# Optimization experiments

Measured on AMD Instinct MI355X. Metric: run time of the kernel, lower is better.

## Reference

```python
import jax, jax.numpy as jnp
import numpy as np

N_LAYER, N_HEAD, D_MODEL, D_FF = 6, 16, 1024, 4096
D_HEAD = D_MODEL // N_HEAD            # 64
M_FEAT = 2 * D_MODEL // N_HEAD        # 128, favor_feature_dims default
CHUNK = 128                           # chunk size for causal linear attention
LN_EPS = 1e-5
ATT_EPS = 1e-6                        # fast-transformers CausalLinearAttention eps
B, S = 4, 2048


def _layer_norm(x, g, b):
    mu = x.mean(-1, keepdims=True)
    var = ((x - mu) ** 2).mean(-1, keepdims=True)
    return (x - mu) * jax.lax.rsqrt(var + LN_EPS) * g + b


def _favor_phi(x, omega):
    # x: [B,H,S,Dh]; omega: [Dh, M//2]. FAVOR positive (hyperbolic) random
    # features: phi(x) = [exp(u - |x|^2/2), exp(-u - |x|^2/2)] / sqrt(M),
    # with x pre-scaled by sqrt(softmax_temp), softmax_temp = 1/sqrt(Dh).
    x = x * (D_HEAD ** -0.25)
    u = jnp.einsum('bhsd,dm->bhsm', x, omega)
    nrm = 0.5 * jnp.sum(x * x, axis=-1, keepdims=True)
    phi = jnp.concatenate([jnp.exp(u - nrm), jnp.exp(-u - nrm)], axis=-1)
    return phi * (M_FEAT ** -0.5)


def _causal_linear_attention(Qp, Kp, V):
    # Qp,Kp: [B,H,S,M] nonnegative features; V: [B,H,S,Dh].
    # out_i = phi(q_i)^T S_i / (phi(q_i)^T Z_i + eps),
    # S_i = sum_{j<=i} phi(k_j) v_j^T, Z_i = sum_{j<=i} phi(k_j).
    # Chunked: exclusive chunk prefix sums + masked intra-chunk matmul.
    b, h, s, m = Qp.shape
    d = V.shape[-1]
    c = s // CHUNK
    Qc = Qp.reshape(b, h, c, CHUNK, m)
    Kc = Kp.reshape(b, h, c, CHUNK, m)
    Vc = V.reshape(b, h, c, CHUNK, d)
    kv = jnp.einsum('bhclm,bhcld->bhcmd', Kc, Vc)   # per-chunk K^T V
    ksum = Kc.sum(axis=3)                            # [b,h,c,m]
    kv_pre = jnp.cumsum(kv, axis=2) - kv             # exclusive prefix over chunks
    ks_pre = jnp.cumsum(ksum, axis=2) - ksum
    scores = jnp.einsum('bhcim,bhcjm->bhcij', Qc, Kc)
    mask = jnp.tril(jnp.ones((CHUNK, CHUNK), bool))
    scores = jnp.where(mask, scores, 0.0)            # causal within chunk
    num = (jnp.einsum('bhcij,bhcjd->bhcid', scores, Vc)
           + jnp.einsum('bhcim,bhcmd->bhcid', Qc, kv_pre))
    den = scores.sum(-1) + jnp.einsum('bhcim,bhcm->bhci', Qc, ks_pre)
    out = num / (den[..., None] + ATT_EPS)
    return out.reshape(b, h, s, d)


def _forward(x, Wq, bq, Wk, bk, Wv, bv, Wo, bo, omega,
             g1, be1, W1, bf1, W2, bf2, g2, be2):
    bsz, slen, _ = x.shape
    out = x
    for l in range(N_LAYER):
        def proj(W, bvec):
            y = jnp.einsum('bsd,de->bse', out, W) + bvec
            return y.reshape(bsz, slen, N_HEAD, D_HEAD).transpose(0, 2, 1, 3)
        q = proj(Wq[l], bq[l])
        k = proj(Wk[l], bk[l])
        v = proj(Wv[l], bv[l])
        Qp = _favor_phi(q, omega[l])
        Kp = _favor_phi(k, omega[l])
        a = _causal_linear_attention(Qp, Kp, v)
        a = a.transpose(0, 2, 1, 3).reshape(bsz, slen, D_MODEL)
        a = jnp.einsum('bsd,de->bse', a, Wo[l]) + bo[l]
        h1 = _layer_norm(out + a, g1[l], be1[l])          # post-norm residual 1
        y = jax.nn.relu(jnp.einsum('bsd,df->bsf', h1, W1[l]) + bf1[l])
        y = jnp.einsum('bsf,fd->bsd', y, W2[l]) + bf2[l]
        out = _layer_norm(h1 + y, g2[l], be2[l])          # post-norm residual 2
    return out


def setup_inputs() -> dict:
    key = jax.random.key(0)
    ks = jax.random.split(key, 12)
    s = D_MODEL ** -0.5
    f32 = jnp.float32
    return {
        "x": jax.random.normal(ks[0], (B, S, D_MODEL), f32),
        "Wq": jax.random.normal(ks[1], (N_LAYER, D_MODEL, D_MODEL), f32) * s,
        "bq": jnp.zeros((N_LAYER, D_MODEL), f32),
        "Wk": jax.random.normal(ks[2], (N_LAYER, D_MODEL, D_MODEL), f32) * s,
        "bk": jnp.zeros((N_LAYER, D_MODEL), f32),
        "Wv": jax.random.normal(ks[3], (N_LAYER, D_MODEL, D_MODEL), f32) * s,
        "bv": jnp.zeros((N_LAYER, D_MODEL), f32),
        "Wo": jax.random.normal(ks[4], (N_LAYER, D_MODEL, D_MODEL), f32) * s,
        "bo": jnp.zeros((N_LAYER, D_MODEL), f32),
        "omega": jax.random.normal(ks[5], (N_LAYER, D_HEAD, M_FEAT // 2), f32),
        "g1": jnp.ones((N_LAYER, D_MODEL), f32),
        "be1": jnp.zeros((N_LAYER, D_MODEL), f32),
        "W1": jax.random.normal(ks[6], (N_LAYER, D_MODEL, D_FF), f32) * s,
        "bf1": jnp.zeros((N_LAYER, D_FF), f32),
        "W2": jax.random.normal(ks[7], (N_LAYER, D_FF, D_MODEL), f32) * (D_FF ** -0.5),
        "bf2": jnp.zeros((N_LAYER, D_MODEL), f32),
        "g2": jnp.ones((N_LAYER, D_MODEL), f32),
        "be2": jnp.zeros((N_LAYER, D_MODEL), f32),
    }


def reference(x, Wq, bq, Wk, bk, Wv, bv, Wo, bo, omega,
              g1, be1, W1, bf1, W2, bf2, g2, be2):
    return _forward(x, Wq, bq, Wk, bk, Wv, bv, Wo, bo, omega,
                    g1, be1, W1, bf1, W2, bf2, g2, be2)
```

## Files before the change

### kernel.cpp

```cpp
#include <hip/hip_runtime.h>

typedef unsigned short u16;
typedef __attribute__((ext_vector_type(8))) short bf16x8;
typedef __attribute__((ext_vector_type(4))) float f32x4;

#define DEV __device__ __forceinline__

DEV float b2f(u16 h){ return __uint_as_float(((unsigned)h) << 16); }
DEV u16 f2b(float f){ unsigned u = __float_as_uint(f); u += 0x7FFFu + ((u >> 16) & 1u); return (u16)(u >> 16); }

DEV void gload16(const u16* g, u16* l){
  __builtin_amdgcn_global_load_lds((const __attribute__((address_space(1))) unsigned*)g,
                                   (__attribute__((address_space(3))) unsigned*)l, 16, 0, 0);
}

__global__ __launch_bounds__(256) void wtrans7(const float* __restrict__ Wq, const float* __restrict__ Wk,
                                               const float* __restrict__ Wv, const float* __restrict__ Wo,
                                               const float* __restrict__ W1, const float* __restrict__ W2,
                                               const float* __restrict__ om,
                                               u16* __restrict__ Wcat, u16* __restrict__ Wot,
                                               u16* __restrict__ W1t, u16* __restrict__ W2t,
                                               u16* __restrict__ omT){
  __shared__ float tile[32][33];
  int id = blockIdx.x;
  const float* src; u16* dst; int K, N, kb, nb; float scale = 1.f;
  if (id < 4096){
    int wsel = id >> 10, loc = id & 1023;
    kb = loc >> 5; nb = loc & 31; K = 1024; N = 1024;
    src = (wsel == 0) ? Wq : (wsel == 1) ? Wk : (wsel == 2) ? Wv : Wo;
    dst = (wsel < 3) ? Wcat + (size_t)wsel * 1048576 : Wot;
  } else if (id < 8192){
    int loc = id - 4096;
    kb = loc & 31; nb = loc >> 5; K = 1024; N = 4096;
    src = W1; dst = W1t;
  } else if (id < 12288){
    int loc = id - 8192;
    kb = loc & 127; nb = loc >> 7; K = 4096; N = 1024;
    src = W2; dst = W2t;
  } else {
    int loc = id - 12288;
    kb = loc & 1; nb = loc >> 1; K = 64; N = 64;
    src = om; dst = omT; scale = 0.35355339059327373f;
  }
  int k0 = kb * 32, n0 = nb * 32;
  int tid = threadIdx.x;
#pragma unroll
  for (int i = 0; i < 4; i++){
    int idx = tid + i * 256;
    int r = idx >> 5, c = idx & 31;
    tile[r][c] = src[(size_t)(k0 + r) * N + n0 + c];
  }
  __syncthreads();
#pragma unroll
  for (int i = 0; i < 4; i++){
    int idx = tid + i * 256;
    int r = idx >> 5, c = idx & 31;
    dst[(size_t)(n0 + r) * K + k0 + c] = f2b(tile[c][r] * scale);
  }
}

__global__ __launch_bounds__(256) void cvt16(const float* __restrict__ src, u16* __restrict__ dst){
  size_t i = ((size_t)blockIdx.x * 256 + threadIdx.x) * 4;
  float4 f = *(const float4*)(src + i);
  ushort4 o = make_ushort4(f2b(f.x), f2b(f.y), f2b(f.z), f2b(f.w));
  *(ushort4*)(dst + i) = o;
}

__global__ void catbias(const float* __restrict__ bq, const float* __restrict__ bk,
                        const float* __restrict__ bv, float* __restrict__ bcat){
  int i = blockIdx.x * 256 + threadIdx.x;
  if (i >= 6 * 3072) return;
  int l = i / 3072, j = i % 3072;
  float v = (j < 1024) ? bq[l * 1024 + j] : (j < 2048) ? bk[l * 1024 + j - 1024] : bv[l * 1024 + j - 2048];
  bcat[i] = v;
}

__global__ void fillv(float* __restrict__ p, float v, int n){
  int i = blockIdx.x * 256 + threadIdx.x;
  if (i < n) p[i] = v;
}

DEV int swz(int r){ return (r & 3) ^ ((r >> 2) & 3); }

template<int EPI>
__global__ __launch_bounds__(256) void gemm_bt(const u16* __restrict__ A, const u16* __restrict__ Bt,
                                               const float* __restrict__ bias, void* __restrict__ outp,
                                               int M, int N, int K, int ldA, int ldB){
  __shared__ __align__(16) u16 As[2][4096];
  __shared__ __align__(16) u16 Bs[2][4096];
  const int tid = threadIdx.x;
  const int lane = tid & 63;
  const int w = tid >> 6;
  const int wm = w >> 1, wn = w & 1;
  int nx = gridDim.x;
  int nwg = nx * gridDim.y;
  int lin = blockIdx.y * nx + blockIdx.x;
  int cpx = nwg >> 3;
  int sw = (lin & 7) * cpx + (lin >> 3);
  const int m0 = (sw / nx) * 128;
  const int n0 = (sw % nx) * 128;

  int r0 = tid >> 2, c0 = tid & 3;
  int r1 = r0 + 64;
  int cs0 = c0 ^ swz(r0);
  int cs1 = c0 ^ swz(r1);
  const u16* ag0 = A + (size_t)(m0 + r0) * ldA + cs0 * 8;
  const u16* ag1 = A + (size_t)(m0 + r1) * ldA + cs1 * 8;
  const u16* bg0 = Bt + (size_t)(n0 + r0) * ldB + cs0 * 8;
  const u16* bg1 = Bt + (size_t)(n0 + r1) * ldB + cs1 * 8;

  f32x4 acc[4][4] = {};
  const int KT = K >> 5;

  gload16(ag0, &As[0][w * 512]);
  gload16(ag1, &As[0][2048 + w * 512]);
  gload16(bg0, &Bs[0][w * 512]);
  gload16(bg1, &Bs[0][2048 + w * 512]);

  for (int kt = 0; kt < KT; kt++){
    int cur = kt & 1;
    if (kt + 1 < KT){
      int ko = (kt + 1) << 5;
      gload16(ag0 + ko, &As[cur ^ 1][w * 512]);
      gload16(ag1 + ko, &As[cur ^ 1][2048 + w * 512]);
      gload16(bg0 + ko, &Bs[cur ^ 1][w * 512]);
      gload16(bg1 + ko, &Bs[cur ^ 1][2048 + w * 512]);
      asm volatile("s_waitcnt vmcnt(4)" ::: "memory");
    } else {
      asm volatile("s_waitcnt vmcnt(0)" ::: "memory");
    }
    __builtin_amdgcn_s_barrier();
    bf16x8 fa[4], fb[4];
#pragma unroll
    for (int m = 0; m < 4; m++){
      int row = wm * 64 + m * 16 + (lane & 15);
      int cc = (lane >> 4) ^ swz(row);
      fa[m] = *(const bf16x8*)(&As[cur][row * 32 + cc * 8]);
    }
#pragma unroll
    for (int n = 0; n < 4; n++){
      int row = wn * 64 + n * 16 + (lane & 15);
      int cc = (lane >> 4) ^ swz(row);
      fb[n] = *(const bf16x8*)(&Bs[cur][row * 32 + cc * 8]);
    }
#pragma unroll
    for (int m = 0; m < 4; m++)
#pragma unroll
      for (int n = 0; n < 4; n++)
        acc[m][n] = __builtin_amdgcn_mfma_f32_16x16x32_bf16(fa[m], fb[n], acc[m][n], 0, 0, 0);
    asm volatile("s_waitcnt lgkmcnt(0)" ::: "memory");
    __builtin_amdgcn_s_barrier();
  }

#pragma unroll
  for (int m = 0; m < 4; m++){
    int rowb = m0 + wm * 64 + m * 16 + ((lane >> 4) << 2);
#pragma unroll
    for (int n = 0; n < 4; n++){
      int col = n0 + wn * 64 + n * 16 + (lane & 15);
      float bv = bias[col];
      if (EPI == 5 && col >= 2048){
        int cv = col - 2048, hh = cv >> 6, dh = cv & 63;
        int bIdx = rowb >> 11, s4 = rowb & 2047;
        ushort4 pk = make_ushort4(f2b(acc[m][n][0] + bv), f2b(acc[m][n][1] + bv),
                                  f2b(acc[m][n][2] + bv), f2b(acc[m][n][3] + bv));
        *(ushort4*)&((u16*)outp + 16777216)[((size_t)(bIdx * 16 + hh) * 64 + dh) * 2048 + s4] = pk;
      } else {
#pragma unroll
        for (int r = 0; r < 4; r++){
          float v = acc[m][n][r] + bv;
          int rr = rowb + r;
          if (EPI == 5){
            u16* dst0 = (u16*)outp + (col < 1024 ? 0 : 8388608);
            int cv = col & 1023, hh = cv >> 6, dh = cv & 63;
            int bIdx = rr >> 11, s = rr & 2047;
            dst0[(((size_t)(bIdx * 16 + hh) * 2048 + s) << 6) + dh] = f2b(v);
          } else if (EPI == 2){
            ((u16*)outp)[(size_t)rr * N + col] = f2b(v > 0.f ? v : 0.f);
          } else {
            ((u16*)outp)[(size_t)rr * N + col] = f2b(v);
          }
        }
      }
    }
  }
}

template<int EPI>
__global__ __launch_bounds__(512, 1) void gemm8p(const u16* __restrict__ A, const u16* __restrict__ Bt,
                                                 const float* __restrict__ bias, void* __restrict__ outp,
                                                 int M, int N, int K, int ldA, int ldB){
  __shared__ __align__(16) u16 As[2][16384];
  __shared__ __align__(16) u16 Bs[2][16384];
  const int tid = threadIdx.x;
  const int lane = tid & 63;
  const int w = tid >> 6;
  const int wm = w >> 2, wn = w & 3;
  int nx = gridDim.x;
  int nwg = nx * gridDim.y;
  int lin = blockIdx.y * nx + blockIdx.x;
  int cpx = nwg >> 3;
  int sw = (lin & 7) * cpx + (lin >> 3);
  const int m0 = (sw / nx) * 256;
  const int n0 = (sw % nx) * 256;

  const int id1 = 512 + tid;
  const int r0 = tid >> 2, c20 = tid & 3;
  const int r1 = id1 >> 2, c21 = id1 & 3;
  const int cs0 = c20 ^ ((r0 >> 1) & 3);
  const int cs1 = c21 ^ ((r1 >> 1) & 3);
  const u16* Ag0 = A + (size_t)(m0 + r0) * ldA + cs0 * 8;
  const u16* Ag1 = A + (size_t)(m0 + r1) * ldA + cs1 * 8;
  const u16* Bg0 = Bt + (size_t)(n0 + r0) * ldB + cs0 * 8;
  const u16* Bg1 = Bt + (size_t)(n0 + r1) * ldB + cs1 * 8;

  f32x4 acc[8][4] = {};
  const int KT = K >> 6;

  auto stA = [&](int buf, int kt, int ks){
    int kc = kt * 64 + ks * 32;
    gload16(Ag0 + kc, &As[buf][ks * 8192 + w * 512]);
    gload16(Ag1 + kc, &As[buf][ks * 8192 + 4096 + w * 512]);
  };
  auto stB = [&](int buf, int kt, int ks){
    int kc = kt * 64 + ks * 32;
    gload16(Bg0 + kc, &Bs[buf][ks * 8192 + w * 512]);
    gload16(Bg1 + kc, &Bs[buf][ks * 8192 + 4096 + w * 512]);
  };

  stA(0, 0, 0); stB(0, 0, 0); stA(0, 0, 1); stB(0, 0, 1);

  for (int t = 0; t < KT; t++){
    int c = t & 1, nb = c ^ 1;
    bool pf = (t + 1 < KT);
    asm volatile("s_waitcnt vmcnt(4)" ::: "memory");
    __builtin_amdgcn_s_barrier();

#pragma unroll
    for (int ks = 0; ks < 2; ks++){
      if (ks == 1){
        if (pf) asm volatile("s_waitcnt vmcnt(4)" ::: "memory");
        else    asm volatile("s_waitcnt vmcnt(0)" ::: "memory");
        __builtin_amdgcn_s_barrier();
      }
      if (pf){ if (ks == 0) stA(nb, t + 1, 0); else stA(nb, t + 1, 1); }
      bf16x8 fa[8], fb[2];
#pragma unroll
      for (int m = 0; m < 8; m++){
        int row = wm * 128 + m * 16 + (lane & 15);
        int slot = (lane >> 4) ^ ((row >> 1) & 3);
        fa[m] = *(const bf16x8*)(&As[c][ks * 8192 + row * 32 + slot * 8]);
      }
#pragma unroll
      for (int nn = 0; nn < 2; nn++){
        int row = wn * 64 + nn * 16 + (lane & 15);
        int slot = (lane >> 4) ^ ((row >> 1) & 3);
        fb[nn] = *(const bf16x8*)(&Bs[c][ks * 8192 + row * 32 + slot * 8]);
      }
      __builtin_amdgcn_s_setprio(1);
#pragma unroll
      for (int m = 0; m < 8; m++)
#pragma unroll
        for (int nn = 0; nn < 2; nn++)
          acc[m][nn] = __builtin_amdgcn_mfma_f32_16x16x32_bf16(fa[m], fb[nn], acc[m][nn], 0, 0, 0);
      __builtin_amdgcn_s_setprio(0);
      if (pf){ if (ks == 0) stB(nb, t + 1, 0); else stB(nb, t + 1, 1); }
#pragma unroll
      for (int nn = 0; nn < 2; nn++){
        int row = wn * 64 + 32 + nn * 16 + (lane & 15);
        int slot = (lane >> 4) ^ ((row >> 1) & 3);
        fb[nn] = *(const bf16x8*)(&Bs[c][ks * 8192 + row * 32 + slot * 8]);
      }
      __builtin_amdgcn_s_setprio(1);
#pragma unroll
      for (int m = 0; m < 8; m++)
#pragma unroll
        for (int nn = 0; nn < 2; nn++)
          acc[m][2 + nn] = __builtin_amdgcn_mfma_f32_16x16x32_bf16(fa[m], fb[nn], acc[m][2 + nn], 0, 0, 0);
      __builtin_amdgcn_s_setprio(0);
    }
  }

#pragma unroll
  for (int m = 0; m < 8; m++){
    int rowb = m0 + wm * 128 + m * 16 + ((lane >> 4) << 2);
#pragma unroll
    for (int n = 0; n < 4; n++){
      int col = n0 + wn * 64 + n * 16 + (lane & 15);
      float bv = bias[col];
#pragma unroll
      for (int r = 0; r < 4; r++){
        float v = acc[m][n][r] + bv;
        int rr = rowb + r;
        if (EPI == 2) ((u16*)outp)[(size_t)rr * N + col] = f2b(v > 0.f ? v : 0.f);
        else          ((u16*)outp)[(size_t)rr * N + col] = f2b(v);
      }
    }
  }
}

__global__ __launch_bounds__(512, 1) void gemm8pk(const u16* __restrict__ A, const u16* __restrict__ Bt,
                                                  const float* __restrict__ bias0, const float* __restrict__ bias1,
                                                  u16* __restrict__ out0, u16* __restrict__ out1,
                                                  int M, int N, int Khalf, int ldA, int ldB){
  __shared__ __align__(16) u16 As[2][16384];
  __shared__ __align__(16) u16 Bs[2][16384];
  const int tid = threadIdx.x;
  const int lane = tid & 63;
  const int w = tid >> 6;
  const int wm = w >> 2, wn = w & 3;
  int lin = blockIdx.x;
  int cpx = gridDim.x >> 3;
  int sw = (lin & 7) * cpx + (lin >> 3);
  const int kz = sw & 1;
  const int t2 = sw >> 1;
  const int n0 = (t2 & 3) * 256;
  const int m0 = (t2 >> 2) * 256;
  const u16* Ab = A + kz * Khalf;
  const u16* Bb = Bt + kz * Khalf;
  u16* outp = kz ? out1 : out0;
  const float* bias = kz ? bias1 : bias0;

  const int id1 = 512 + tid;
  const int r0 = tid >> 2, c20 = tid & 3;
  const int r1 = id1 >> 2, c21 = id1 & 3;
  const int cs0 = c20 ^ ((r0 >> 1) & 3);
  const int cs1 = c21 ^ ((r1 >> 1) & 3);
  const u16* Ag0 = Ab + (size_t)(m0 + r0) * ldA + cs0 * 8;
  const u16* Ag1 = Ab + (size_t)(m0 + r1) * ldA + cs1 * 8;
  const u16* Bg0 = Bb + (size_t)(n0 + r0) * ldB + cs0 * 8;
  const u16* Bg1 = Bb + (size_t)(n0 + r1) * ldB + cs1 * 8;

  f32x4 acc[8][4] = {};
  const int KT = Khalf >> 6;

  auto stA = [&](int buf, int kt, int ks){
    int kc = kt * 64 + ks * 32;
    gload16(Ag0 + kc, &As[buf][ks * 8192 + w * 512]);
    gload16(Ag1 + kc, &As[buf][ks * 8192 + 4096 + w * 512]);
  };
  auto stB = [&](int buf, int kt, int ks){
    int kc = kt * 64 + ks * 32;
    gload16(Bg0 + kc, &Bs[buf][ks * 8192 + w * 512]);
    gload16(Bg1 + kc, &Bs[buf][ks * 8192 + 4096 + w * 512]);
  };

  stA(0, 0, 0); stB(0, 0, 0); stA(0, 0, 1); stB(0, 0, 1);

  for (int t = 0; t < KT; t++){
    int c = t & 1, nb = c ^ 1;
    bool pf = (t + 1 < KT);
    asm volatile("s_waitcnt vmcnt(4)" ::: "memory");
    __builtin_amdgcn_s_barrier();

#pragma unroll
    for (int ks = 0; ks < 2; ks++){
      if (ks == 1){
        if (pf) asm volatile("s_waitcnt vmcnt(4)" ::: "memory");
        else    asm volatile("s_waitcnt vmcnt(0)" ::: "memory");
        __builtin_amdgcn_s_barrier();
      }
      if (pf){ if (ks == 0) stA(nb, t + 1, 0); else stA(nb, t + 1, 1); }
      bf16x8 fa[8], fb[2];
#pragma unroll
      for (int m = 0; m < 8; m++){
        int row = wm * 128 + m * 16 + (lane & 15);
        int slot = (lane >> 4) ^ ((row >> 1) & 3);
        fa[m] = *(const bf16x8*)(&As[c][ks * 8192 + row * 32 + slot * 8]);
      }
#pragma unroll
      for (int nn = 0; nn < 2; nn++){
        int row = wn * 64 + nn * 16 + (lane & 15);
        int slot = (lane >> 4) ^ ((row >> 1) & 3);
        fb[nn] = *(const bf16x8*)(&Bs[c][ks * 8192 + row * 32 + slot * 8]);
      }
      __builtin_amdgcn_s_setprio(1);
#pragma unroll
      for (int m = 0; m < 8; m++)
#pragma unroll
        for (int nn = 0; nn < 2; nn++)
          acc[m][nn] = __builtin_amdgcn_mfma_f32_16x16x32_bf16(fa[m], fb[nn], acc[m][nn], 0, 0, 0);
      __builtin_amdgcn_s_setprio(0);
      if (pf){ if (ks == 0) stB(nb, t + 1, 0); else stB(nb, t + 1, 1); }
#pragma unroll
      for (int nn = 0; nn < 2; nn++){
        int row = wn * 64 + 32 + nn * 16 + (lane & 15);
        int slot = (lane >> 4) ^ ((row >> 1) & 3);
        fb[nn] = *(const bf16x8*)(&Bs[c][ks * 8192 + row * 32 + slot * 8]);
      }
      __builtin_amdgcn_s_setprio(1);
#pragma unroll
      for (int m = 0; m < 8; m++)
#pragma unroll
        for (int nn = 0; nn < 2; nn++)
          acc[m][2 + nn] = __builtin_amdgcn_mfma_f32_16x16x32_bf16(fa[m], fb[nn], acc[m][2 + nn], 0, 0, 0);
      __builtin_amdgcn_s_setprio(0);
    }
  }

#pragma unroll
  for (int m = 0; m < 8; m++){
    int rowb = m0 + wm * 128 + m * 16 + ((lane >> 4) << 2);
#pragma unroll
    for (int n = 0; n < 4; n++){
      int col = n0 + wn * 64 + n * 16 + (lane & 15);
      float bv = bias[col];
#pragma unroll
      for (int r = 0; r < 4; r++)
        outp[(size_t)(rowb + r) * N + col] = f2b(acc[m][n][r] + bv);
    }
  }
}

__global__ __launch_bounds__(256) void phi2(const u16* __restrict__ qb, const u16* __restrict__ kb,
                                            const u16* __restrict__ omT,
                                            u16* __restrict__ Qp, u16* __restrict__ Kp){
  __shared__ __align__(16) u16 qs[128 * 64];
  __shared__ __align__(16) u16 wl[64 * 64];
  __shared__ __align__(16) u16 ph[128 * 128];
  __shared__ float part[2][128];
  __shared__ float nrm[128];
  int tid = threadIdx.x, w = tid >> 6, lane = tid & 63;
  int blk = blockIdx.x;
  const u16* src; u16* dst; int row0;
  if (blk < 1024){ src = qb; dst = Qp; row0 = blk * 128; }
  else           { src = kb; dst = Kp; row0 = (blk - 1024) * 128; }
  const u16* g = src + (size_t)row0 * 64;
#pragma unroll
  for (int i = 0; i < 4; i++){
    int id = tid * 4 + i;
    int r = id >> 3, kc = id & 7;
    *(bf16x8*)(qs + r * 64 + ((kc ^ (r & 7)) << 3)) = *(const bf16x8*)(g + r * 64 + kc * 8);
  }
#pragma unroll
  for (int i = 0; i < 2; i++){
    int id = tid * 2 + i;
    int m = id >> 3, kc = id & 7;
    *(bf16x8*)(wl + m * 64 + ((kc ^ (m & 7)) << 3)) = *(const bf16x8*)(omT + id * 8);
  }
  __syncthreads();
  {
    int r = tid & 127, half = tid >> 7;
    float s = 0.f;
#pragma unroll
    for (int j = 0; j < 4; j++){
      int kc = half * 4 + j;
      bf16x8 v = *(const bf16x8*)(qs + r * 64 + ((kc ^ (r & 7)) << 3));
#pragma unroll
      for (int e = 0; e < 8; e++){ float f = b2f((u16)v[e]); s += f * f; }
    }
    part[half][r] = s;
  }
  __syncthreads();
  if (tid < 128) nrm[tid] = 0.0625f * (part[0][tid] + part[1][tid]);
  __syncthreads();
  f32x4 acc[2][4] = {};
#pragma unroll
  for (int kt = 0; kt < 2; kt++){
    int kc = kt * 4 + (lane >> 4);
    bf16x8 fa[2], fb[4];
#pragma unroll
    for (int mt = 0; mt < 2; mt++){
      int r = w * 32 + mt * 16 + (lane & 15);
      fa[mt] = *(const bf16x8*)(qs + r * 64 + ((kc ^ (r & 7)) << 3));
    }
#pragma unroll
    for (int nt = 0; nt < 4; nt++){
      int m = nt * 16 + (lane & 15);
      fb[nt] = *(const bf16x8*)(wl + m * 64 + ((kc ^ (m & 7)) << 3));
    }
#pragma unroll
    for (int mt = 0; mt < 2; mt++)
#pragma unroll
      for (int nt = 0; nt < 4; nt++)
        acc[mt][nt] = __builtin_amdgcn_mfma_f32_16x16x32_bf16(fa[mt], fb[nt], acc[mt][nt], 0, 0, 0);
  }
  const float LNC = -2.4260151319598086f;
#pragma unroll
  for (int mt = 0; mt < 2; mt++)
#pragma unroll
    for (int nt = 0; nt < 4; nt++)
#pragma unroll
      for (int r4 = 0; r4 < 4; r4++){
        int r = w * 32 + mt * 16 + ((lane >> 4) << 2) + r4;
        int m = nt * 16 + (lane & 15);
        float u = acc[mt][nt][r4];
        float nr = nrm[r];
        ph[r * 128 + m]      = f2b(__expf(u - nr + LNC));
        ph[r * 128 + 64 + m] = f2b(__expf(-u - nr + LNC));
      }
  __syncthreads();
  u16* go = dst + (size_t)row0 * 128;
#pragma unroll
  for (int i = 0; i < 8; i++){
    int id = i * 256 + tid;
    *(bf16x8*)(go + id * 8) = *(const bf16x8*)(ph + id * 8);
  }
}

__global__ __launch_bounds__(256) void kvchunk(const u16* __restrict__ Kp, const u16* __restrict__ vt,
                                               u16* __restrict__ kv, float* __restrict__ ksum){
  __shared__ __align__(16) u16 Ks[128 * 128];
  __shared__ __align__(16) u16 Vst[64 * 128];
  int blk = blockIdx.x; int bh = blk >> 4, c = blk & 15;
  int tid = threadIdx.x;
  size_t base = (size_t)bh * 2048 + c * 128;
  const u16* Kc = Kp + base * 128;
  const u16* vtc = vt + (size_t)bh * 64 * 2048 + c * 128;
  {
    int j = tid >> 1, half = tid & 1;
#pragma unroll
    for (int i = 0; i < 8; i++)
      *(bf16x8*)(Ks + j * 128 + half * 64 + i * 8) = *(const bf16x8*)(Kc + j * 128 + half * 64 + i * 8);
#pragma unroll
    for (int i = 0; i < 4; i++){
      int id = tid * 4 + i;
      int d = id >> 4, mc = id & 15;
      *(bf16x8*)(Vst + d * 128 + mc * 8) = *(const bf16x8*)(vtc + (size_t)d * 2048 + mc * 8);
    }
  }
  __syncthreads();
  int tm = tid & 15, td = tid >> 4;
  int mbase = tm * 8, dbase = td * 4;
  float acc[8][4] = {};
  float ks[8] = {};
  for (int i = 0; i < 128; i++){
    bf16x8 kk = *(const bf16x8*)(Ks + i * 128 + mbase);
    float kf[8];
#pragma unroll
    for (int e = 0; e < 8; e++) kf[e] = b2f((u16)kk[e]);
    float vf[4];
#pragma unroll
    for (int e = 0; e < 4; e++) vf[e] = b2f(Vst[(dbase + e) * 128 + i]);
#pragma unroll
    for (int a = 0; a < 8; a++){
      ks[a] += kf[a];
#pragma unroll
      for (int bb = 0; bb < 4; bb++) acc[a][bb] += kf[a] * vf[bb];
    }
  }
  u16* kvout = kv + ((size_t)bh * 16 + c) * 8192;
#pragma unroll
  for (int a = 0; a < 8; a++)
#pragma unroll
    for (int bb = 0; bb < 4; bb++)
      kvout[(size_t)(dbase + bb) * 128 + mbase + a] = f2b(acc[a][bb]);
  if (td == 0){
    float* kso = ksum + ((size_t)bh * 16 + c) * 128;
#pragma unroll
    for (int a = 0; a < 8; a++) kso[mbase + a] = ks[a];
  }
}

__global__ __launch_bounds__(256) void kvscan(u16* __restrict__ kv, float* __restrict__ ksum){
  int bh = blockIdx.x;
  int p = blockIdx.y;
  int tid = threadIdx.x;
  if (p < 8){
    size_t base = (size_t)bh * 16 * 8192;
    int idx0 = p * 1024 + tid;
    for (int rep = 0; rep < 4; rep++){
      int idx = idx0 + rep * 256;
      float run = 0.f;
#pragma unroll
      for (int c = 0; c < 16; c++){
        size_t off = base + (size_t)c * 8192 + idx;
        float v = b2f(kv[off]); kv[off] = f2b(run); run += v;
      }
    }
  } else if (tid < 128){
    size_t base = (size_t)bh * 16 * 128;
    float run = 0.f;
#pragma unroll
    for (int c = 0; c < 16; c++){
      size_t off = base + c * 128 + tid;
      float v = ksum[off]; ksum[off] = run; run += v;
    }
  }
}

__global__ __launch_bounds__(512) void attn_fused(const u16* __restrict__ Qp, const u16* __restrict__ Kp,
                                                  const u16* __restrict__ vt, const u16* __restrict__ kvp,
                                                  const float* __restrict__ ksum, u16* __restrict__ aout){
  __shared__ __align__(16) u16 sm[53248];
  int blk = blockIdx.x, bh = blk >> 4, c = blk & 15;
  int b = bh >> 4, h = bh & 15;
  int tid = threadIdx.x, w = tid >> 6, lane = tid & 63;
  size_t base = (size_t)bh * 2048 + c * 128;
  const u16* Qc = Qp + base * 128;
  const u16* Kc = Kp + base * 128;
  const u16* vtc = vt + (size_t)bh * 64 * 2048 + c * 128;
  const u16* kvc = kvp + ((size_t)bh * 16 + c) * 8192;
  const float* ksc = ksum + ((size_t)bh * 16 + c) * 128;
  u16* Qs = sm;
  u16* Ks = sm + 16384;
  u16* B2 = sm + 32768;

#pragma unroll
  for (int i = 0; i < 4; i++){
    int id = tid * 4 + i;
    int r = id >> 4, kc = id & 15;
    int swo = (kc ^ (r & 15)) << 3;
    *(bf16x8*)(Qs + r * 128 + swo) = *(const bf16x8*)(Qc + (size_t)r * 128 + kc * 8);
    *(bf16x8*)(Ks + r * 128 + swo) = *(const bf16x8*)(Kc + (size_t)r * 128 + kc * 8);
  }
#pragma unroll
  for (int i = 0; i < 2; i++){
    int id = tid * 2 + i;
    int d = id >> 4, kc = id & 15;
    *(bf16x8*)(B2 + d * 256 + ((kc ^ (d & 31)) << 3)) = *(const bf16x8*)(vtc + (size_t)d * 2048 + kc * 8);
  }
#pragma unroll
  for (int i = 0; i < 2; i++){
    int id = tid * 2 + i;
    int d = id >> 4, mc = id & 15;
    bf16x8 pk = *(const bf16x8*)(kvc + d * 128 + mc * 8);
    int kc = 16 + mc;
    *(bf16x8*)(B2 + d * 256 + ((kc ^ (d & 31)) << 3)) = pk;
  }
  {
    int row = 64 + (tid >> 5), kc = tid & 31;
    bf16x8 pk = {};
    if (row == 64){
      if (kc < 16){
#pragma unroll
        for (int e = 0; e < 8; e++) pk[e] = (short)0x3F80;
      } else {
        const float* s8 = ksc + (kc - 16) * 8;
        float4 f0 = *(const float4*)(s8);
        float4 f1 = *(const float4*)(s8 + 4);
        pk[0] = (short)f2b(f0.x); pk[1] = (short)f2b(f0.y); pk[2] = (short)f2b(f0.z); pk[3] = (short)f2b(f0.w);
        pk[4] = (short)f2b(f1.x); pk[5] = (short)f2b(f1.y); pk[6] = (short)f2b(f1.z); pk[7] = (short)f2b(f1.w);
      }
    }
    *(bf16x8*)(B2 + row * 256 + ((kc ^ (row & 31)) << 3)) = pk;
  }
  __syncthreads();

  int wm = w >> 2, wn = w & 3;
  f32x4 acc1[4][2] = {};
#pragma unroll
  for (int kk = 0; kk < 4; kk++){
    int kc = kk * 4 + (lane >> 4);
    bf16x8 fa[4], fb[2];
#pragma unroll
    for (int m = 0; m < 4; m++){
      int row = wm * 64 + m * 16 + (lane & 15);
      fa[m] = *(const bf16x8*)(Qs + row * 128 + ((kc ^ (row & 15)) << 3));
    }
#pragma unroll
    for (int n = 0; n < 2; n++){
      int row = wn * 32 + n * 16 + (lane & 15);
      fb[n] = *(const bf16x8*)(Ks + row * 128 + ((kc ^ (row & 15)) << 3));
    }
#pragma unroll
    for (int m = 0; m < 4; m++)
#pragma unroll
      for (int n = 0; n < 2; n++)
        acc1[m][n] = __builtin_amdgcn_mfma_f32_16x16x32_bf16(fa[m], fb[n], acc1[m][n], 0, 0, 0);
  }
  __syncthreads();

#pragma unroll
  for (int m = 0; m < 4; m++)
#pragma unroll
    for (int n = 0; n < 2; n++)
#pragma unroll
      for (int r = 0; r < 4; r++){
        int i = wm * 64 + m * 16 + ((lane >> 4) << 2) + r;
        int j = wn * 32 + n * 16 + (lane & 15);
        float v = (j <= i) ? acc1[m][n][r] : 0.f;
        Ks[i * 128 + (((j >> 3) ^ (i & 15)) << 3) + (j & 7)] = f2b(v);
      }
  __syncthreads();

  f32x4 acc2[5] = {};
#pragma unroll
  for (int kk = 0; kk < 8; kk++){
    int kc = kk * 4 + (lane >> 4);
    int rowA = w * 16 + (lane & 15);
    bf16x8 fa2;
    if (kk < 4) fa2 = *(const bf16x8*)(Ks + rowA * 128 + ((kc ^ (rowA & 15)) << 3));
    else        fa2 = *(const bf16x8*)(Qs + rowA * 128 + (((kc - 16) ^ (rowA & 15)) << 3));
#pragma unroll
    for (int n = 0; n < 5; n++){
      int d = n * 16 + (lane & 15);
      bf16x8 fb2 = *(const bf16x8*)(B2 + d * 256 + ((kc ^ (d & 31)) << 3));
      acc2[n] = __builtin_amdgcn_mfma_f32_16x16x32_bf16(fa2, fb2, acc2[n], 0, 0, 0);
    }
  }

  float dd[4];
#pragma unroll
  for (int r = 0; r < 4; r++) dd[r] = __shfl(acc2[4][r], lane & 48) + 1e-6f;
  size_t obase = ((size_t)b * 2048 + c * 128) * 1024 + (size_t)h * 64;
#pragma unroll
  for (int n = 0; n < 4; n++)
#pragma unroll
    for (int r = 0; r < 4; r++){
      int i = w * 16 + ((lane >> 4) << 2) + r;
      int d = n * 16 + (lane & 15);
      aout[obase + (size_t)i * 1024 + d] = f2b(acc2[n][r] / dd[r]);
    }
}

__global__ __launch_bounds__(256) void lnr(const float* X1f, const u16* X1b,
                                           const u16* P0, const u16* P1,
                                           const float* __restrict__ g, const float* __restrict__ bb,
                                           float* outf, u16* outb, u16* outb2){
  __shared__ float red[2][4];
  int row = blockIdx.x, tid = threadIdx.x, w = tid >> 6, lane = tid & 63;
  size_t ro = (size_t)row * 1024 + tid * 4;
  float x0, x1, x2, x3;
  if (X1f){
    float4 a = *(const float4*)(X1f + ro);
    x0 = a.x; x1 = a.y; x2 = a.z; x3 = a.w;
  } else {
    ushort4 a = *(const ushort4*)(X1b + ro);
    x0 = b2f(a.x); x1 = b2f(a.y); x2 = b2f(a.z); x3 = b2f(a.w);
  }
  {
    ushort4 p0 = *(const ushort4*)(P0 + ro);
    x0 += b2f(p0.x); x1 += b2f(p0.y); x2 += b2f(p0.z); x3 += b2f(p0.w);
  }
  if (P1){
    ushort4 p1 = *(const ushort4*)(P1 + ro);
    x0 += b2f(p1.x); x1 += b2f(p1.y); x2 += b2f(p1.z); x3 += b2f(p1.w);
  }
  float s1 = x0 + x1 + x2 + x3;
  float s2 = x0 * x0 + x1 * x1 + x2 * x2 + x3 * x3;
#pragma unroll
  for (int off = 32; off; off >>= 1){ s1 += __shfl_xor(s1, off); s2 += __shfl_xor(s2, off); }
  if (lane == 0){ red[0][w] = s1; red[1][w] = s2; }
  __syncthreads();
  float t1 = red[0][0] + red[0][1] + red[0][2] + red[0][3];
  float t2 = red[1][0] + red[1][1] + red[1][2] + red[1][3];
  float mu = t1 * (1.f / 1024.f);
  float var = t2 * (1.f / 1024.f) - mu * mu;
  float rs = rsqrtf(var + 1e-5f);
  float4 gv = *(const float4*)(g + tid * 4);
  float4 bv = *(const float4*)(bb + tid * 4);
  float o0 = (x0 - mu) * rs * gv.x + bv.x;
  float o1 = (x1 - mu) * rs * gv.y + bv.y;
  float o2 = (x2 - mu) * rs * gv.z + bv.z;
  float o3 = (x3 - mu) * rs * gv.w + bv.w;
  if (outf) *(float4*)(outf + ro) = make_float4(o0, o1, o2, o3);
  ushort4 ob = make_ushort4(f2b(o0), f2b(o1), f2b(o2), f2b(o3));
  if (outb)  *(ushort4*)(outb + ro)  = ob;
  if (outb2) *(ushort4*)(outb2 + ro) = ob;
}

extern "C" void kernel_launch(void* const* d_in, const int* in_sizes, int n_in,
                              void* d_out, int out_size, void* d_ws, size_t ws_size,
                              hipStream_t stream){
  (void)in_sizes; (void)n_in;
  const float* x   = (const float*)d_in[0];
  const float* Wq  = (const float*)d_in[1];
  const float* bq  = (const float*)d_in[2];
  const float* Wk  = (const float*)d_in[3];
  const float* bk  = (const float*)d_in[4];
  const float* Wv  = (const float*)d_in[5];
  const float* bv  = (const float*)d_in[6];
  const float* Wo  = (const float*)d_in[7];
  const float* bo  = (const float*)d_in[8];
  const float* om  = (const float*)d_in[9];
  const float* g1  = (const float*)d_in[10];
  const float* be1 = (const float*)d_in[11];
  const float* W1  = (const float*)d_in[12];
  const float* bf1 = (const float*)d_in[13];
  const float* W2  = (const float*)d_in[14];
  const float* bf2 = (const float*)d_in[15];
  const float* g2  = (const float*)d_in[16];
  const float* be2 = (const float*)d_in[17];

  char* ws = (char*)d_ws;
  size_t off = 0;
  auto alloc = [&](size_t bytes) -> void* {
    void* p = ws + off; off += (bytes + 255) & ~(size_t)255; return p;
  };
  u16* Wcat = (u16*)alloc(3072ull * 1024 * 2);
  u16* Wot  = (u16*)alloc(1024ull * 1024 * 2);
  u16* W1t  = (u16*)alloc(4096ull * 1024 * 2);
  u16* W2t  = (u16*)alloc(1024ull * 4096 * 2);
  u16* omT  = (u16*)alloc(64ull * 64 * 2);
  float* bcat = (float*)alloc(6ull * 3072 * 4);
  float* zbuf = (float*)alloc(1024 * 4);
  u16* Xb  = (u16*)alloc(8192ull * 1024 * 2);
  u16* qb  = (u16*)alloc(131072ull * 64 * 2);
  u16* kb  = (u16*)alloc(131072ull * 64 * 2);
  u16* vt  = (u16*)alloc(131072ull * 64 * 2);
  u16* Qp  = (u16*)alloc(131072ull * 128 * 2);
  u16* Kp  = (u16*)alloc(131072ull * 128 * 2);
  float* ksum = (float*)alloc(64ull * 16 * 128 * 4);

  if (off > ws_size){
    fillv<<<(out_size + 255) / 256, 256, 0, stream>>>((float*)d_out, (float)(ws_size >> 20), out_size);
    return;
  }

  u16*  kvbuf  = qb;
  u16*  ybuf   = qb;
  u16*  wooutb = Qp;
  u16*  w2outb = Qp + 8388608;
  u16*  w2p1   = Kp + 8388608;
  u16*  residb = (u16*)d_out;

  cvt16<<<8192, 256, 0, stream>>>(x, Xb);
  catbias<<<72, 256, 0, stream>>>(bq, bk, bv, bcat);
  fillv<<<4, 256, 0, stream>>>(zbuf, 0.f, 1024);

  for (int l = 0; l < 6; l++){
    size_t o1k = (size_t)l * 1024 * 1024;
    size_t o4k = (size_t)l * 4096 * 1024;
    wtrans7<<<12292, 256, 0, stream>>>(Wq + o1k, Wk + o1k, Wv + o1k, Wo + o1k,
                                       W1 + o4k, W2 + o4k, om + (size_t)l * 4096,
                                       Wcat, Wot, W1t, W2t, omT);

    gemm_bt<5><<<dim3(24, 64), 256, 0, stream>>>(Xb, Wcat, bcat + l * 3072, qb, 8192, 3072, 1024, 1024, 1024);
    phi2<<<2048, 256, 0, stream>>>(qb, kb, omT, Qp, Kp);
    kvchunk<<<1024, 256, 0, stream>>>(Kp, vt, kvbuf, ksum);
    kvscan<<<dim3(64, 9), 256, 0, stream>>>(kvbuf, ksum);
    attn_fused<<<1024, 512, 0, stream>>>(Qp, Kp, vt, kvbuf, ksum, Xb);
    gemm_bt<6><<<dim3(8, 64), 256, 0, stream>>>(Xb, Wot, bo + l * 1024, wooutb, 8192, 1024, 1024, 1024, 1024);
    lnr<<<8192, 256, 0, stream>>>(l == 0 ? x : nullptr, l == 0 ? nullptr : residb,
                                  wooutb, nullptr, g1 + l * 1024, be1 + l * 1024,
                                  nullptr, Xb, nullptr);
    gemm8p<2><<<dim3(16, 32), 512, 0, stream>>>(Xb, W1t, bf1 + l * 4096, ybuf, 8192, 4096, 1024, 1024, 1024);
    gemm8pk<<<dim3(256), 512, 0, stream>>>(ybuf, W2t, bf2 + l * 1024, zbuf, w2outb, w2p1,
                                           8192, 1024, 2048, 4096, 4096);
    if (l == 5)
      lnr<<<8192, 256, 0, stream>>>(nullptr, Xb, w2outb, w2p1, g2 + l * 1024, be2 + l * 1024,
                                    (float*)d_out, nullptr, nullptr);
    else
      lnr<<<8192, 256, 0, stream>>>(nullptr, Xb, w2outb, w2p1, g2 + l * 1024, be2 + l * 1024,
                                    nullptr, Xb, residb);
  }
}
```

Before: 2.411 ms.

## Fuse per-chunk K^T V and key-sum computation into the phi feature kernel

The K-branch blocks of phi2 now also load the matching V chunk and compute that chunk's K^T V product and key feature sum from the phi values already held in shared memory. This removes the separate kvchunk launch and its re-read of Kp from global memory. A dedicated kv buffer is allocated when workspace allows, and the old path remains as a fallback. The fused product uses scalar FMA loops instead of MFMA, and the extra shared memory may reduce phi2 occupancy, so the added tail work on K blocks could offset the saved launch.

```diff
diff --git a/kernel.cpp b/kernel.cpp
--- a/kernel.cpp
+++ b/kernel.cpp
@@ -414,17 +414,21 @@
 
 __global__ __launch_bounds__(256) void phi2(const u16* __restrict__ qb, const u16* __restrict__ kb,
                                             const u16* __restrict__ omT,
-                                            u16* __restrict__ Qp, u16* __restrict__ Kp){
+                                            u16* __restrict__ Qp, u16* __restrict__ Kp,
+                                            const u16* __restrict__ vt,
+                                            u16* __restrict__ kv, float* __restrict__ ksum, int fuse){
   __shared__ __align__(16) u16 qs[128 * 64];
   __shared__ __align__(16) u16 wl[64 * 64];
   __shared__ __align__(16) u16 ph[128 * 128];
+  __shared__ __align__(16) u16 Vst[64 * 128];
   __shared__ float part[2][128];
   __shared__ float nrm[128];
   int tid = threadIdx.x, w = tid >> 6, lane = tid & 63;
   int blk = blockIdx.x;
   const u16* src; u16* dst; int row0;
-  if (blk < 1024){ src = qb; dst = Qp; row0 = blk * 128; }
-  else           { src = kb; dst = Kp; row0 = (blk - 1024) * 128; }
+  bool isK = (blk >= 1024);
+  if (!isK){ src = qb; dst = Qp; row0 = blk * 128; }
+  else     { src = kb; dst = Kp; row0 = (blk - 1024) * 128; }
   const u16* g = src + (size_t)row0 * 64;
 #pragma unroll
   for (int i = 0; i < 4; i++){
@@ -489,12 +493,56 @@
         ph[r * 128 + m]      = f2b(__expf(u - nr + LNC));
         ph[r * 128 + 64 + m] = f2b(__expf(-u - nr + LNC));
       }
+  int bh = 0, cch = 0;
+  if (isK && fuse){
+    int rr0 = blk - 1024;
+    bh = rr0 >> 4; cch = rr0 & 15;
+    const u16* vtc = vt + (size_t)bh * 131072 + cch * 128;
+#pragma unroll
+    for (int i = 0; i < 4; i++){
+      int id = tid * 4 + i;
+      int d = id >> 4, mc = id & 15;
+      *(bf16x8*)(Vst + d * 128 + mc * 8) = *(const bf16x8*)(vtc + (size_t)d * 2048 + mc * 8);
+    }
+  }
   __syncthreads();
   u16* go = dst + (size_t)row0 * 128;
 #pragma unroll
   for (int i = 0; i < 8; i++){
     int id = i * 256 + tid;
     *(bf16x8*)(go + id * 8) = *(const bf16x8*)(ph + id * 8);
+  }
+  if (isK && fuse){
+    int tm = tid & 15, td = tid >> 4;
+    int mbase = tm * 8, dbase = td * 4;
+    float acc2[8][4] = {};
+    float ks[8] = {};
+    for (int i = 0; i < 128; i++){
+      bf16x8 kk = *(const bf16x8*)(ph + i * 128 + mbase);
+      float kf[8];
+#pragma unroll
+      for (int e = 0; e < 8; e++) kf[e] = b2f((u16)kk[e]);
+      float vf[4];
+#pragma unroll
+      for (int e = 0; e < 4; e++) vf[e] = b2f(Vst[(dbase + e) * 128 + i]);
+#pragma unroll
+      for (int a = 0; a < 8; a++){
+        ks[a] += kf[a];
+#pragma unroll
+        for (int bb = 0; bb < 4; bb++) acc2[a][bb] += kf[a] * vf[bb];
+      }
+    }
+    u16* kvout = kv + ((size_t)bh * 16 + cch) * 8192;
+#pragma unroll
+    for (int a = 0; a < 8; a++)
+#pragma unroll
+      for (int bb = 0; bb < 4; bb++)
+        kvout[(size_t)(dbase + bb) * 128 + mbase + a] = f2b(acc2[a][bb]);
+    if (td == 0){
+      float* kso = ksum + ((size_t)bh * 16 + cch) * 128;
+#pragma unroll
+      for (int a = 0; a < 8; a++) kso[mbase + a] = ks[a];
+    }
   }
 }
 
@@ -792,13 +840,17 @@
   u16* Qp  = (u16*)alloc(131072ull * 128 * 2);
   u16* Kp  = (u16*)alloc(131072ull * 128 * 2);
   float* ksum = (float*)alloc(64ull * 16 * 128 * 4);
+  size_t base_end = off;
+
+  u16* kvded = (u16*)alloc(64ull * 16 * 8192 * 2);
+  bool fuse = (off <= ws_size);
+  if (!fuse){ off = base_end; kvded = qb; }
 
   if (off > ws_size){
     fillv<<<(out_size + 255) / 256, 256, 0, stream>>>((float*)d_out, (float)(ws_size >> 20), out_size);
     return;
   }
 
-  u16*  kvbuf  = qb;
   u16*  ybuf   = qb;
   u16*  wooutb = Qp;
   u16*  w2outb = Qp + 8388608;
@@ -817,10 +869,10 @@
                                        Wcat, Wot, W1t, W2t, omT);
 
     gemm_bt<5><<<dim3(24, 64), 256, 0, stream>>>(Xb, Wcat, bcat + l * 3072, qb, 8192, 3072, 1024, 1024, 1024);
-    phi2<<<2048, 256, 0, stream>>>(qb, kb, omT, Qp, Kp);
-    kvchunk<<<1024, 256, 0, stream>>>(Kp, vt, kvbuf, ksum);
-    kvscan<<<dim3(64, 9), 256, 0, stream>>>(kvbuf, ksum);
-    attn_fused<<<1024, 512, 0, stream>>>(Qp, Kp, vt, kvbuf, ksum, Xb);
+    phi2<<<2048, 256, 0, stream>>>(qb, kb, omT, Qp, Kp, vt, kvded, ksum, fuse ? 1 : 0);
+    if (!fuse) kvchunk<<<1024, 256, 0, stream>>>(Kp, vt, kvded, ksum);
+    kvscan<<<dim3(64, 9), 256, 0, stream>>>(kvded, ksum);
+    attn_fused<<<1024, 512, 0, stream>>>(Qp, Kp, vt, kvded, ksum, Xb);
     gemm_bt<6><<<dim3(8, 64), 256, 0, stream>>>(Xb, Wot, bo + l * 1024, wooutb, 8192, 1024, 1024, 1024, 1024);
     lnr<<<8192, 256, 0, stream>>>(l == 0 ? x : nullptr, l == 0 ? nullptr : residb,
                                   wooutb, nullptr, g1 + l * 1024, be1 + l * 1024,
```

Result: no change. 2.379 ms (-1.4%).
